# Kernel tuning notes

Hardware: AMD Instinct MI355X
Metric: run time of the kernel (lower is better)

Reference implementation:

```python
import jax, jax.numpy as jnp
import numpy as np

H = 32; L = 4; HEADS = 8; VC = 16; BIG = 1e9

def _unit(v):
    return v * jax.lax.rsqrt(jnp.sum(v * v, -1, keepdims=True) + 1e-8)

def _dihedrals(bb):
    n = bb.shape[0]
    X = bb[:, :3].reshape(n * 3, 3)
    U = _unit(X[1:] - X[:-1])
    u2, u1, u0 = U[:-2], U[1:-1], U[2:]
    n2 = _unit(jnp.cross(u2, u1)); n1 = _unit(jnp.cross(u1, u0))
    cosD = jnp.clip(jnp.sum(n2 * n1, -1), -1 + 1e-6, 1 - 1e-6)
    D = jnp.sign(jnp.sum(u2 * n1, -1)) * jnp.arccos(cosD)
    D = jnp.pad(D, (1, 2)).reshape(n, 3)
    return jnp.concatenate([jnp.cos(D), jnp.sin(D)], -1)

def _orientations(x):
    f = jnp.pad(_unit(x[1:] - x[:-1]), ((0, 1), (0, 0)))
    b = jnp.pad(_unit(x[:-1] - x[1:]), ((1, 0), (0, 0)))
    return jnp.stack([f, b], -2)

def _virtual_cb(bb):
    n_, ca, c = bb[:, 0], bb[:, 1], bb[:, 2]
    b = ca - n_; cc = c - ca; a = jnp.cross(b, cc)
    return -0.58273431 * a + 0.56802827 * b - 0.54067466 * cc + ca

def _rbf(d, nbin=16, dmax=20.0):
    mu = jnp.linspace(0.0, dmax, nbin); sig = dmax / nbin
    return jnp.exp(-(((d[..., None] - mu) / sig) ** 2))

def _pos_emb(didx, nemb=16):
    freq = jnp.exp(jnp.arange(0, nemb, 2, dtype=jnp.float32) * (-np.log(10000.0) / nemb))
    ang = didx[..., None].astype(jnp.float32) * freq
    return jnp.concatenate([jnp.cos(ang), jnp.sin(ang)], -1)

def _edge_rot(vec):
    # per-edge rotation aligning edge direction to e_y (equiformer-style)
    nrm = _unit(vec)
    helper = jnp.where(jnp.abs(nrm[..., 2:3]) > 0.99, jnp.array([1.0, 0.0, 0.0]), jnp.array([0.0, 0.0, 1.0]))
    z = _unit(jnp.cross(nrm, helper))
    x = jnp.cross(nrm, z)
    return jnp.stack([x, nrm, z], axis=-2)

def _rot(R, x):
    return jnp.concatenate([x[..., :1, :], jnp.einsum('...ij,...jc->...ic', R, x[..., 1:, :])], -2)

def _rot_inv(R, x):
    return jnp.concatenate([x[..., :1, :], jnp.einsum('...ji,...jc->...ic', R, x[..., 1:, :])], -2)

def _norm_so3(x, g0, b0, g1):
    x0 = x[..., 0, :]; x1 = x[..., 1:, :]
    mu = jnp.mean(x0, -1, keepdims=True)
    var = jnp.var(x0, -1, keepdims=True)
    y0 = (x0 - mu) * jax.lax.rsqrt(var + 1e-6) * g0 + b0
    y1 = x1 * jax.lax.rsqrt(jnp.mean(x1 * x1, (-2, -1), keepdims=True) + 1e-6) * g1
    return jnp.concatenate([y0[..., None, :], y1], -2)

def _project(xin, nbr, R, ef, rw1, rw2, ow):
    src = _rot(R, xin[nbr])                         # [N,k,4,Cin] gather + rotate into edge frame
    rad = jax.nn.silu(ef @ rw1) @ rw2               # [N,k,Cin] radial weights
    msg = _rot_inv(R, src * rad[..., None, :])      # rotate back to global frame
    return jnp.mean(msg, axis=1) @ ow               # [N,4,Cout]

def _forward(bb, latent, ln_g0, ln_b0, ln_g1, bb_rad_w1, bb_rad_w2, bb_out_w,
             lat_rad_w1, lat_rad_w2, lat_out_w, tln_g0, tln_b0, tln_g1,
             attn_w1, attn_w2, v_w, o_w, ffn_w1, ffn_w2, ffn_wg, ffn_v1,
             eu_w1, eu_w2, out_rad_w1, out_rad_w2, out_w,
             seq_w1, seq_b1, seq_w2, seq_b2, seq_w3, seq_b3, x_mask, n_per, k):
    N = bb.shape[0]
    Xca = bb[:, 1]
    # backbone SO3 features [N,4,7]: l=0 dihedrals (padded to 7), l=1 seven vectors
    dih = jnp.pad(_dihedrals(bb), ((0, 0), (0, 1)))
    vecs = jnp.concatenate([bb - Xca[:, None], _orientations(Xca),
                            (_virtual_cb(bb) - Xca)[:, None]], -2)
    bb_feat = jnp.concatenate([dih[:, None, :], jnp.nan_to_num(jnp.swapaxes(vecs, -1, -2))], 1)
    # kNN graph within each chain; masked residues pushed far away
    batch = jnp.arange(N) // n_per
    mx = jnp.where(x_mask[:, None], BIG, Xca)
    sq = jnp.sum(mx * mx, -1)
    d2 = sq[:, None] + sq[None, :] - 2.0 * (mx @ mx.T)
    bad = (batch[:, None] != batch[None, :]) | jnp.eye(N, dtype=bool)
    d2 = jnp.where(bad, BIG, d2)
    _, nbr = jax.lax.top_k(-d2, k)                  # [N,k] source indices per target
    edge_vec = Xca[:, None] - Xca[nbr]
    R = _edge_rot(edge_vec)                         # [N,k,3,3]
    dist = jnp.sqrt(jnp.sum(edge_vec * edge_vec, -1) + 1e-12)
    ef = jnp.concatenate([_rbf(dist), _pos_emb(nbr - jnp.arange(N)[:, None])], -1)  # [N,k,32]
    lat = _norm_so3(latent, ln_g0, ln_b0, ln_g1)
    x = jnp.concatenate([_project(bb_feat, nbr, R, ef, bb_rad_w1, bb_rad_w2, bb_out_w),
                         _project(lat, nbr, R, ef, lat_rad_w1, lat_rad_w2, lat_out_w)], -1)  # [N,4,H]
    for l in range(L):
        xl = _norm_so3(x, tln_g0[l], tln_b0[l], tln_g1[l])
        src = xl[nbr]                               # [N,k,4,H]
        feat = jnp.concatenate([src[..., 0, :],
                                jnp.broadcast_to(xl[:, None, 0, :], src[..., 0, :].shape),
                                ef], -1)            # [N,k,3H]
        alpha = jax.nn.softmax(jax.nn.silu(feat @ attn_w1[l]) @ attn_w2[l], axis=1)  # [N,k,heads]
        v = _rot_inv(R, _rot(R, src) @ v_w[l])      # [N,k,4,heads*vc]
        v = v.reshape(N, k, 4, HEADS, VC)
        agg = jnp.einsum('nkh,nkchv->nchv', alpha, v).reshape(N, 4, HEADS * VC)
        x = x + agg @ o_w[l]
        h = jax.nn.silu(x[:, 0, :] @ ffn_w1[l])
        gate = jax.nn.sigmoid(h @ ffn_wg[l])
        x = x + jnp.concatenate([(h @ ffn_w2[l])[:, None, :],
                                 (x[:, 1:, :] @ ffn_v1[l]) * gate[:, None, :]], 1)
        e_in = jnp.concatenate([ef, x[nbr][..., 0, :],
                                jnp.broadcast_to(x[:, None, 0, :], (N, k, H))], -1)
        ef = ef + jax.nn.silu(e_in @ eu_w1[l]) @ eu_w2[l]
    atoms = _project(x, nbr, R, ef, out_rad_w1, out_rad_w2, out_w)  # [N,4,91]
    decoded_latent = jnp.swapaxes(atoms[:, 1:4, :], -1, -2)         # [N,91,3]
    hh = jax.nn.relu(x[:, 0, :] @ seq_w1 + seq_b1)
    hh = jax.nn.relu(hh @ seq_w2 + seq_b2)
    seq_logits = jax.nn.log_softmax(hh @ seq_w3 + seq_b3, -1)
    return decoded_latent, seq_logits

def setup_inputs() -> dict:
    key = jax.random.key(0)
    N = 8192; n_per = 2048; k = 30
    keys = iter(jax.random.split(key, 64))
    def W(shape):
        fan = shape[-2] if len(shape) > 1 else shape[-1]
        return (jax.random.normal(next(keys), shape) / np.sqrt(fan)).astype(jnp.float32)
    inp = {
        'bb': (jax.random.normal(next(keys), (N, 4, 3)) * 3.0).astype(jnp.float32),
        'latent': jax.random.normal(next(keys), (N, 4, H), dtype=jnp.float32),
        'ln_g0': jnp.ones((H,), jnp.float32), 'ln_b0': jnp.zeros((H,), jnp.float32), 'ln_g1': jnp.ones((H,), jnp.float32),
        'bb_rad_w1': W((H, 64)), 'bb_rad_w2': W((64, 7)), 'bb_out_w': W((7, 16)),
        'lat_rad_w1': W((H, 64)), 'lat_rad_w2': W((64, H)), 'lat_out_w': W((H, 16)),
        'tln_g0': jnp.ones((L, H), jnp.float32), 'tln_b0': jnp.zeros((L, H), jnp.float32), 'tln_g1': jnp.ones((L, H), jnp.float32),
        'attn_w1': W((L, 3 * H, H)), 'attn_w2': W((L, H, HEADS)),
        'v_w': W((L, H, HEADS * VC)), 'o_w': W((L, HEADS * VC, H)),
        'ffn_w1': W((L, H, 2 * H)), 'ffn_w2': W((L, 2 * H, H)), 'ffn_wg': W((L, 2 * H, H)), 'ffn_v1': W((L, H, H)),
        'eu_w1': W((L, 3 * H, 2 * H)), 'eu_w2': W((L, 2 * H, H)),
        'out_rad_w1': W((H, 64)), 'out_rad_w2': W((64, H)), 'out_w': W((H, 91)),
        'seq_w1': W((H, 64)), 'seq_b1': jnp.zeros((64,), jnp.float32),
        'seq_w2': W((64, H)), 'seq_b2': jnp.zeros((H,), jnp.float32),
        'seq_w3': W((H, 20)), 'seq_b3': jnp.zeros((20,), jnp.float32),
        'x_mask': jnp.zeros((N,), bool), 'n_per': n_per, 'k': k,
    }
    return inp

def reference(bb, latent, ln_g0, ln_b0, ln_g1, bb_rad_w1, bb_rad_w2, bb_out_w,
              lat_rad_w1, lat_rad_w2, lat_out_w, tln_g0, tln_b0, tln_g1,
              attn_w1, attn_w2, v_w, o_w, ffn_w1, ffn_w2, ffn_wg, ffn_v1,
              eu_w1, eu_w2, out_rad_w1, out_rad_w2, out_w,
              seq_w1, seq_b1, seq_w2, seq_b2, seq_w3, seq_b3, x_mask, n_per, k):
    return _forward(bb, latent, ln_g0, ln_b0, ln_g1, bb_rad_w1, bb_rad_w2, bb_out_w,
                    lat_rad_w1, lat_rad_w2, lat_out_w, tln_g0, tln_b0, tln_g1,
                    attn_w1, attn_w2, v_w, o_w, ffn_w1, ffn_w2, ffn_wg, ffn_v1,
                    eu_w1, eu_w2, out_rad_w1, out_rad_w2, out_w,
                    seq_w1, seq_b1, seq_w2, seq_b2, seq_w3, seq_b3, x_mask, n_per, k)
```

## Files before the change

### kernel.cpp

```cpp
#include <hip/hip_runtime.h>
#include <math.h>

#define NRES 8192
#define NPER 2048
#define KNB  30
#define NEDGE (NRES*KNB)

typedef float v2f __attribute__((ext_vector_type(2)));

__device__ __forceinline__ float siluf(float x){ return x / (1.0f + __expf(-x)); }
__device__ __forceinline__ v2f splat2(float a){ v2f r; r.x=a; r.y=a; return r; }

__global__ void k_bbfeat(const float* __restrict__ bb, float* __restrict__ bbf,
                         float4* __restrict__ ca){
  int n = blockIdx.x*256 + threadIdx.x;
  if(n >= NRES) return;
  const float* r = bb + n*12;
  float cax=r[3], cay=r[4], caz=r[5];
  ca[n] = make_float4(cax,cay,caz, cax*cax+cay*cay+caz*caz);
  float vx[7],vy[7],vz[7];
  for(int a=0;a<4;a++){ vx[a]=r[a*3]-cax; vy[a]=r[a*3+1]-cay; vz[a]=r[a*3+2]-caz; }
  if(n<NRES-1){
    float dx=bb[(n+1)*12+3]-cax, dy=bb[(n+1)*12+4]-cay, dz=bb[(n+1)*12+5]-caz;
    float s=rsqrtf(dx*dx+dy*dy+dz*dz+1e-8f);
// ... 83 lines not shown
    if(j==il) d2 = 1e30f;
    vals[t]=d2;
  }
  unsigned mask = 0;
  unsigned long long s0 = knn_extract(vals, mask, lane);
  unsigned long long s1 = knn_extract(vals, mask, lane);
  unsigned long long s2 = knn_extract(vals, mask, lane);
  unsigned long long s3 = knn_extract(vals, mask, lane);
  const unsigned long long EMPTY = ~0ull;
  for(int it=0; it<KNB; it++){
    unsigned long long m = s0;
    #pragma unroll
    for(int off=32; off>0; off>>=1){
      unsigned long long o = __shfl_xor(m, off, 64);
      m = (o<m) ? o : m;
    }
    if(lane==0) nbr[i*KNB+it] = base + (int)(m & 0x7FFull);
    if((int)(m & 63ull) == lane){
      s0=s1; s1=s2; s2=s3; s3=EMPTY;
      if(s0==EMPTY) s0 = knn_extract(vals, mask, lane);
    }
  }
}

__global__ void k_tbl(float* __restrict__ tbl){
  int i = blockIdx.x*256 + threadIdx.x;
  int d = i>>3, m = i&7;
  float freq = __expf(-1.1512925465f*(float)m);
  float ang = (float)(d-2048)*freq;
  tbl[d*16+m]   = cosf(ang);
  tbl[d*16+8+m] = sinf(ang);
}

__global__ void k_edgefeat(const float4* __restrict__ ca, const int* __restrict__ nbr,
                           const float* __restrict__ tbl, float* __restrict__ ef){
  int e = blockIdx.x*256 + threadIdx.x;
  if(e >= NEDGE) return;
  int n = e/KNB;
  int j = nbr[e];
  float4 cn = ca[n], cj = ca[j];
  float dx=cn.x-cj.x, dy=cn.y-cj.y, dz=cn.z-cj.z;
  float dist = sqrtf(dx*dx+dy*dy+dz*dz + 1e-12f);
  float f[32];
  #pragma unroll
  for(int m=0;m<16;m++){
    float mu = (20.0f/15.0f)*(float)m;
    float t = (dist-mu)*(1.0f/1.25f);
    f[m] = __expf(-t*t);
  }
  {
    const float4* t4 = (const float4*)(tbl + (size_t)(j - n + 2048)*16);
    float4 c0=t4[0], c1=t4[1], s0=t4[2], s1=t4[3];
    f[16]=c0.x; f[17]=c0.y; f[18]=c0.z; f[19]=c0.w;
    f[20]=c1.x; f[21]=c1.y; f[22]=c1.z; f[23]=c1.w;
    f[24]=s0.x; f[25]=s0.y; f[26]=s0.z; f[27]=s0.w;
    f[28]=s1.x; f[29]=s1.y; f[30]=s1.z; f[31]=s1.w;
  }
  float4* o4 = (float4*)(ef + (size_t)e*32);
  #pragma unroll
  for(int q=0;q<8;q++) o4[q] = make_float4(f[q*4],f[q*4+1],f[q*4+2],f[q*4+3]);
}

__global__ void k_norm(const float* __restrict__ in, float* __restrict__ out,
                       const float* __restrict__ g0, const float* __restrict__ b0,
                       const float* __restrict__ g1){
  int tid = blockIdx.x*256 + threadIdx.x;
  int n = tid >> 5, lane = tid & 31;
  if(n >= NRES) return;
  const float* xn = in + n*128;
  float x0 = xn[lane];
  float s = x0, s2 = x0*x0;
  for(int off=16; off>0; off>>=1){ s += __shfl_xor(s, off, 32); s2 += __shfl_xor(s2, off, 32); }
  float mu = s*(1.0f/32.0f);
  float var = s2*(1.0f/32.0f) - mu*mu;
  float y0 = (x0-mu)*rsqrtf(var+1e-6f)*g0[lane] + b0[lane];
  float v1 = xn[32+lane], v2 = xn[64+lane], v3 = xn[96+lane];
  float ss = v1*v1+v2*v2+v3*v3;
  for(int off=16; off>0; off>>=1){ ss += __shfl_xor(ss, off, 32); }
  float sc = rsqrtf(ss*(1.0f/96.0f) + 1e-6f);
  float g = g1[lane];
  out[n*128+lane]     = y0;
  out[n*128+32+lane]  = v1*sc*g;
  out[n*128+64+lane]  = v2*sc*g;
  out[n*128+96+lane]  = v3*sc*g;
}

__device__ __forceinline__ void load32(float* __restrict__ f, const float* __restrict__ src){
  const float4* s4 = (const float4*)src;
  #pragma unroll
  for(int q=0;q<8;q++){
    float4 v = s4[q];
    f[q*4+0]=v.x; f[q*4+1]=v.y; f[q*4+2]=v.z; f[q*4+3]=v.w;
  }
}

__global__ __launch_bounds__(128, 4)
void k_rad(const float* __restrict__ ef,
           const float* __restrict__ bbw1, const float* __restrict__ bbw2,
           const float* __restrict__ latw1, const float* __restrict__ latw2,
           float* __restrict__ radbb, float* __restrict__ radlat){
  int e = blockIdx.x*128 + threadIdx.x;
  float f[32];
  load32(f, ef + (size_t)e*32);
  float ab[7];
  #pragma unroll
  for(int t=0;t<7;t++) ab[t]=0.f;
  #pragma unroll
  for(int half=0; half<2; half++){
    v2f h[16];
    #pragma unroll
    for(int o=0;o<16;o++) h[o]=splat2(0.f);
    #pragma unroll
    for(int c=0;c<32;c++){
      v2f fc = splat2(f[c]);
      const v2f* w = (const v2f*)(bbw1 + c*64 + half*32);
      #pragma unroll
      for(int o=0;o<16;o++) h[o] += fc*w[o];
    }
    #pragma unroll
    for(int o=0;o<16;o++){
      float v0 = siluf(h[o].x), v1 = siluf(h[o].y);
      const float* wa = bbw2 + (half*32+o*2)*7;
      const float* wb = bbw2 + (half*32+o*2+1)*7;
      #pragma unroll
      for(int t=0;t<7;t++) ab[t] += v0*wa[t];
      #pragma unroll
      for(int t=0;t<7;t++) ab[t] += v1*wb[t];
    }
  }
  {
    float4* rb4 = (float4*)(radbb + (size_t)e*8);
    rb4[0] = make_float4(ab[0],ab[1],ab[2],ab[3]);
    rb4[1] = make_float4(ab[4],ab[5],ab[6],0.f);
  }
  v2f al[16];
  #pragma unroll
  for(int t=0;t<16;t++) al[t]=splat2(0.f);
  #pragma unroll
  for(int half=0; half<2; half++){
    v2f h[16];
    #pragma unroll
    for(int o=0;o<16;o++) h[o]=splat2(0.f);
    #pragma unroll
    for(int c=0;c<32;c++){
      v2f fc = splat2(f[c]);
      const v2f* w = (const v2f*)(latw1 + c*64 + half*32);
      #pragma unroll
      for(int o=0;o<16;o++) h[o] += fc*w[o];
    }
    #pragma unroll
    for(int o=0;o<16;o++){
      float v0 = siluf(h[o].x), v1 = siluf(h[o].y);
      const v2f* wa = (const v2f*)(latw2 + (half*32+o*2)*32);
      const v2f* wb = (const v2f*)(latw2 + (half*32+o*2+1)*32);
      v2f va = splat2(v0), vb = splat2(v1);
      #pragma unroll
      for(int t=0;t<16;t++) al[t] += va*wa[t];
      #pragma unroll
      for(int t=0;t<16;t++) al[t] += vb*wb[t];
    }
  }
  v2f* rl2 = (v2f*)(radlat + (size_t)e*32);
  #pragma unroll
  for(int q=0;q<16;q++) rl2[q] = al[q];
}

__global__ __launch_bounds__(256) void k_init(const int* __restrict__ nbr,
                       const float* __restrict__ radbb, const float* __restrict__ radlat,
                       const float* __restrict__ bbf, const float* __restrict__ latn,
                       const float* __restrict__ bboutw, const float* __restrict__ latoutw,
                       const float* __restrict__ g0, const float* __restrict__ b0,
                       const float* __restrict__ g1,
                       float* __restrict__ x, float* __restrict__ xl){
  __shared__ float msgbb[4][32], msglat[4][128], xout[4][128];
  int g = threadIdx.x>>6, t = threadIdx.x&63;
  int n = blockIdx.x*4 + g;
  int t31 = t&31, t7 = t%7;
  float accL0=0.f, accL1=0.f, accB=0.f;
  for(int kk=0; kk<KNB; kk++){
    int e = n*KNB+kk;
    int j = nbr[e];
    float rl = radlat[(size_t)e*32 + t31];
    accL0 += latn[j*128+t]    * rl;
    accL1 += latn[j*128+64+t] * rl;
    if(t<28) accB += bbf[j*28+t]*radbb[(size_t)e*8 + t7];
  }
  msglat[g][t]=accL0*(1.0f/KNB); msglat[g][64+t]=accL1*(1.0f/KNB);
  if(t<28) msgbb[g][t]=accB*(1.0f/KNB);
  for(int half=0; half<2; half++){
    int e = half*64+t;
    int rrow = e>>5, c = e&31;
    float v=0.f;
    if(c<16){ for(int q=0;q<7;q++)  v += msgbb[g][rrow*7+q]*bboutw[q*16+c]; }
    else    { for(int q=0;q<32;q++) v += msglat[g][rrow*32+q]*latoutw[q*16+(c-16)]; }
    xout[g][e]=v;
    x[n*128+e]=v;
  }
  if(t<32){
    float x0=xout[g][t];
    float s=x0, s2=x0*x0;
    for(int off=16; off>0; off>>=1){ s+=__shfl_xor(s,off,32); s2+=__shfl_xor(s2,off,32); }
    float mu=s*(1.0f/32.0f), var=s2*(1.0f/32.0f)-mu*mu;
    float y0=(x0-mu)*rsqrtf(var+1e-6f)*g0[t]+b0[t];
    float v1=xout[g][32+t], v2=xout[g][64+t], v3=xout[g][96+t];
    float ss=v1*v1+v2*v2+v3*v3;
    for(int off=16; off>0; off>>=1) ss+=__shfl_xor(ss,off,32);
    float sc=rsqrtf(ss*(1.0f/96.0f)+1e-6f);
    float gg=g1[t];
    xl[n*128+t]=y0; xl[n*128+32+t]=v1*sc*gg; xl[n*128+64+t]=v2*sc*gg; xl[n*128+96+t]=v3*sc*gg;
  }
}

__global__ __launch_bounds__(256) void k_nodeprep(const float* __restrict__ x,
                       const float* __restrict__ xl,
                       const float* __restrict__ ew1, const float* __restrict__ aw1,
                       float* __restrict__ hsrc, float* __restrict__ hdst,
                       float* __restrict__ asrc, float* __restrict__ adst){
  __shared__ float sx[4][32], sl[4][32];
  int g = threadIdx.x>>6, lane = threadIdx.x&63;
  int n = blockIdx.x*4 + g;
  if(lane<32){
    if(x)   sx[g][lane] = x[n*128+lane];
    if(aw1) sl[g][lane] = xl[n*128+lane];
  }
  __syncthreads();
  if(x){
    float a0=0.f, a1=0.f;
    #pragma unroll
    for(int c=0;c<32;c++){
      float xv = sx[g][c];
      a0 += xv*ew1[(32+c)*64+lane];
      a1 += xv*ew1[(64+c)*64+lane];
    }
    hsrc[n*64+lane]=a0; hdst[n*64+lane]=a1;
  }
  if(aw1){
    int o = lane&31;
    int roff = (lane>=32)? 32 : 0;
    float a=0.f;
    #pragma unroll
    for(int c=0;c<32;c++) a += sl[g][c]*aw1[(roff+c)*32+o];
    if(lane<32) asrc[n*32+o]=a; else adst[n*32+o]=a;
  }
}

__global__ __launch_bounds__(128, 4)
void k_logits(const int* __restrict__ nbr,
              const float* __restrict__ asrc, const float* __restrict__ adst,
              const float* __restrict__ ef, const float* __restrict__ w1,
              const float* __restrict__ w2, float* __restrict__ logits){
  int e = blockIdx.x*128 + threadIdx.x;
  int n = e/KNB;
  int j = nbr[e];
  v2f h[16];
  {
    const v2f* pj = (const v2f*)(asrc + (size_t)j*32);
    const v2f* pn = (const v2f*)(adst + (size_t)n*32);
    #pragma unroll
    for(int q=0;q<16;q++) h[q] = pj[q]+pn[q];
  }
  float f[32];
  load32(f, ef + (size_t)e*32);
  #pragma unroll
  for(int c=0;c<32;c++){
    v2f fc = splat2(f[c]);
    const v2f* w = (const v2f*)(w1 + (64+c)*32);
    #pragma unroll
    for(int o=0;o<16;o++) h[o] += fc*w[o];
  }
  v2f acc[4];
  #pragma unroll
  for(int t=0;t<4;t++) acc[t]=splat2(0.f);
  #pragma unroll
  for(int o=0;o<16;o++){
    float v0 = siluf(h[o].x), v1 = siluf(h[o].y);
    const v2f* wa = (const v2f*)(w2 + (o*2)*8);
    const v2f* wb = (const v2f*)(w2 + (o*2+1)*8);
    v2f va = splat2(v0), vb = splat2(v1);
    #pragma unroll
    for(int t=0;t<4;t++) acc[t] += va*wa[t];
    #pragma unroll
    for(int t=0;t<4;t++) acc[t] += vb*wb[t];
  }
  v2f* lg2 = (v2f*)(logits + (size_t)e*8);
  #pragma unroll
  for(int q=0;q<4;q++) lg2[q] = acc[q];
}

__global__ __launch_bounds__(256) void k_update(const int* __restrict__ nbr, const float* __restrict__ xl,
                         const float* __restrict__ logits, float* __restrict__ x,
                         float* __restrict__ xlout,
                         const float* __restrict__ vw, const float* __restrict__ ow,
                         const float* __restrict__ fw1, const float* __restrict__ fw2,
                         const float* __restrict__ fwg, const float* __restrict__ fv1,
                         const float* __restrict__ g0, const float* __restrict__ b0,
                         const float* __restrict__ g1){
  __shared__ float S_lg[4][240], S_m[4][8], S_inv[4][8];
  __shared__ float S_S[4][1024], S_agg[4][512], S_x[4][128];
  __shared__ float S_h[4][64], S_g[4][32], S_d0[4][32];
  int g = threadIdx.x>>6, t = threadIdx.x&63;
  int n = blockIdx.x*4 + g;
  for(int r=t; r<240; r+=64) S_lg[g][r] = logits[(size_t)n*240+r];
  if(t<8){
    float m=-1e30f;
    for(int kk=0;kk<KNB;kk++) m=fmaxf(m, S_lg[g][kk*8+t]);
    float s=0.f;
    for(int kk=0;kk<KNB;kk++) s += __expf(S_lg[g][kk*8+t]-m);
    S_m[g][t]=m; S_inv[g][t]=1.0f/s;
  }
  for(int r=t; r<240; r+=64){ int h=r&7; S_lg[g][r]=__expf(S_lg[g][r]-S_m[g][h])*S_inv[g][h]; }
  int hd = t>>3, i8 = t&7;
  v2f acc[8];
  #pragma unroll
  for(int m=0;m<8;m++) acc[m]=splat2(0.f);
  for(int kk=0;kk<KNB;kk++){
    int j=nbr[n*KNB+kk];
    v2f a = splat2(S_lg[g][kk*8+hd]);
    const v2f* xr = (const v2f*)(xl + (size_t)j*128 + i8*16);
    #pragma unroll
    for(int q=0;q<8;q++) acc[q] += a*xr[q];
  }
  #pragma unroll
  for(int q=0;q<8;q++){ S_S[g][hd*128 + i8*16 + 2*q] = acc[q].x; S_S[g][hd*128 + i8*16 + 2*q+1] = acc[q].y; }
  __syncthreads();
  for(int half=0; half<2; half++){
    int hv = half*64+t;
    int hh = hv>>4;
    v2f a01=splat2(0.f), a23=splat2(0.f);
    for(int c=0;c<32;c++){
      v2f w = splat2(vw[c*128+hv]);
      v2f s01; s01.x = S_S[g][hh*128 + c];      s01.y = S_S[g][hh*128 + 32+c];
      v2f s23; s23.x = S_S[g][hh*128 + 64+c];   s23.y = S_S[g][hh*128 + 96+c];
      a01 += s01*w; a23 += s23*w;
    }
    S_agg[g][hv]=a01.x; S_agg[g][128+hv]=a01.y; S_agg[g][256+hv]=a23.x; S_agg[g][384+hv]=a23.y;
  }
  __syncthreads();
  {
    int c = t&31, r0 = t>>5;
    v2f v01; v01.x = x[n*128+t]; v01.y = x[n*128+64+t];
    for(int hv=0;hv<128;hv++){
      v2f s; s.x = S_agg[g][r0*128+hv]; s.y = S_agg[g][(r0+2)*128+hv];
      v01 += s*splat2(ow[hv*32+c]);
    }
    S_x[g][t]=v01.x; S_x[g][64+t]=v01.y;
  }
  __syncthreads();
  {
    float hs=0.f;
    for(int c=0;c<32;c++) hs += S_x[g][c]*fw1[c*64+t];
    S_h[g][t]=siluf(hs);
  }
  __syncthreads();
  if(t<32){
    float gs=0.f, d0=0.f;
    for(int c=0;c<64;c++){ float hv=S_h[g][c]; gs += hv*fwg[c*32+t]; d0 += hv*fw2[c*32+t]; }
    S_g[g][t]=1.0f/(1.0f+__expf(-gs));
    S_d0[g][t]=d0;
  }
  __syncthreads();
  for(int half=0; half<2; half++){
    int e = half*64+t;
    int rrow = e>>5, c = e&31;
    float xv = S_x[g][e], outv;
    if(rrow==0){ outv = xv + S_d0[g][c]; }
    else {
      float dv=0.f;
      for(int cc=0;cc<32;cc++) dv += S_x[g][rrow*32+cc]*fv1[cc*32+c];
      outv = xv + dv*S_g[g][c];
    }
    __syncthreads();
    S_x[g][e]=outv;
    x[n*128+e]=outv;
  }
  __syncthreads();
  if(t<32){
    float x0=S_x[g][t];
    float s=x0, s2=x0*x0;
    for(int off=16; off>0; off>>=1){ s+=__shfl_xor(s,off,32); s2+=__shfl_xor(s2,off,32); }
    float mu=s*(1.0f/32.0f), var=s2*(1.0f/32.0f)-mu*mu;
    float y0=(x0-mu)*rsqrtf(var+1e-6f)*g0[t]+b0[t];
    float v1=S_x[g][32+t], v2=S_x[g][64+t], v3=S_x[g][96+t];
    float ss=v1*v1+v2*v2+v3*v3;
    for(int off=16; off>0; off>>=1) ss+=__shfl_xor(ss,off,32);
    float sc=rsqrtf(ss*(1.0f/96.0f)+1e-6f);
    float gg=g1[t];
    xlout[n*128+t]=y0; xlout[n*128+32+t]=v1*sc*gg;
    xlout[n*128+64+t]=v2*sc*gg; xlout[n*128+96+t]=v3*sc*gg;
  }
}

template<bool FUSE_LOGITS>
__global__ __launch_bounds__(128, 4)
void k_efup_t(const int* __restrict__ nbr,
              const float* __restrict__ hsrc, const float* __restrict__ hdst,
              const float* __restrict__ ew1, const float* __restrict__ ew2,
              float* __restrict__ ef,
              const float* __restrict__ asrc, const float* __restrict__ adst,
              const float* __restrict__ aw1n, const float* __restrict__ aw2n,
              float* __restrict__ logits){
  int e = blockIdx.x*128 + threadIdx.x;
  int n = e/KNB;
  int j = nbr[e];
  float f[32];
  load32(f, ef + (size_t)e*32);
  v2f acc[16];
  #pragma unroll
  for(int t=0;t<16;t++) acc[t]=splat2(0.f);
  #pragma unroll
  for(int half=0; half<2; half++){
    v2f h[16];
    {
      const v2f* pj = (const v2f*)(hsrc + (size_t)j*64 + half*32);
      const v2f* pn = (const v2f*)(hdst + (size_t)n*64 + half*32);
      #pragma unroll
      for(int q=0;q<16;q++) h[q] = pj[q]+pn[q];
    }
    #pragma unroll
    for(int c=0;c<32;c++){
      v2f fc = splat2(f[c]);
      const v2f* w = (const v2f*)(ew1 + c*64 + half*32);
      #pragma unroll
      for(int o=0;o<16;o++) h[o] += fc*w[o];
    }
    #pragma unroll
    for(int o=0;o<16;o++){
      float v0 = siluf(h[o].x), v1 = siluf(h[o].y);
      const v2f* wa = (const v2f*)(ew2 + (half*32+o*2)*32);
      const v2f* wb = (const v2f*)(ew2 + (half*32+o*2+1)*32);
      v2f va = splat2(v0), vb = splat2(v1);
      #pragma unroll
      for(int t=0;t<16;t++) acc[t] += va*wa[t];
      #pragma unroll
      for(int t=0;t<16;t++) acc[t] += vb*wb[t];
    }
  }
  #pragma unroll
  for(int t=0;t<16;t++){ f[2*t] += acc[t].x; f[2*t+1] += acc[t].y; }
  float4* e4 = (float4*)(ef + (size_t)e*32);
  #pragma unroll
  for(int q=0;q<8;q++)
    e4[q] = make_float4(f[q*4+0], f[q*4+1], f[q*4+2], f[q*4+3]);
  if(FUSE_LOGITS){
    v2f h2[16];
    {
      const v2f* pj = (const v2f*)(asrc + (size_t)j*32);
      const v2f* pn = (const v2f*)(adst + (size_t)n*32);
      #pragma unroll
      for(int q=0;q<16;q++) h2[q] = pj[q]+pn[q];
    }
    #pragma unroll
    for(int c=0;c<32;c++){
      v2f fc = splat2(f[c]);
      const v2f* w = (const v2f*)(aw1n + (64+c)*32);
      #pragma unroll
      for(int o=0;o<16;o++) h2[o] += fc*w[o];
    }
    v2f a8[4];
    #pragma unroll
    for(int t=0;t<4;t++) a8[t]=splat2(0.f);
    #pragma unroll
    for(int o=0;o<16;o++){
      float v0 = siluf(h2[o].x), v1 = siluf(h2[o].y);
      const v2f* wa = (const v2f*)(aw2n + (o*2)*8);
      const v2f* wb = (const v2f*)(aw2n + (o*2+1)*8);
      v2f va = splat2(v0), vb = splat2(v1);
      #pragma unroll
      for(int t=0;t<4;t++) a8[t] += va*wa[t];
      #pragma unroll
      for(int t=0;t<4;t++) a8[t] += vb*wb[t];
    }
    v2f* lg2 = (v2f*)(logits + (size_t)e*8);
    #pragma unroll
    for(int q=0;q<4;q++) lg2[q] = a8[q];
  }
}

__global__ __launch_bounds__(128, 4)
void k_orad(const float* __restrict__ ef,
            const float* __restrict__ orw1, const float* __restrict__ orw2,
            float* __restrict__ orad){
  int e = blockIdx.x*128 + threadIdx.x;
  float f[32];
  load32(f, ef + (size_t)e*32);
  v2f acc[16];
  #pragma unroll
  for(int t=0;t<16;t++) acc[t]=splat2(0.f);
  #pragma unroll
  for(int half=0; half<2; half++){
    v2f h[16];
    #pragma unroll
    for(int o=0;o<16;o++) h[o]=splat2(0.f);
    #pragma unroll
    for(int c=0;c<32;c++){
      v2f fc = splat2(f[c]);
      const v2f* w = (const v2f*)(orw1 + c*64 + half*32);
      #pragma unroll
      for(int o=0;o<16;o++) h[o] += fc*w[o];
    }
    #pragma unroll
    for(int o=0;o<16;o++){
      float v0 = siluf(h[o].x), v1 = siluf(h[o].y);
      const v2f* wa = (const v2f*)(orw2 + (half*32+o*2)*32);
      const v2f* wb = (const v2f*)(orw2 + (half*32+o*2+1)*32);
      v2f va = splat2(v0), vb = splat2(v1);
      #pragma unroll
      for(int t=0;t<16;t++) acc[t] += va*wa[t];
      #pragma unroll
      for(int t=0;t<16;t++) acc[t] += vb*wb[t];
    }
  }
  v2f* r2 = (v2f*)(orad + (size_t)e*32);
  #pragma unroll
  for(int q=0;q<16;q++) r2[q] = acc[q];
}

__global__ __launch_bounds__(256) void k_out(const int* __restrict__ nbr, const float* __restrict__ orad,
                      const float* __restrict__ x,
                      const float* __restrict__ outw,
                      const float* __restrict__ sw1, const float* __restrict__ sb1,
                      const float* __restrict__ sw2, const float* __restrict__ sb2,
                      const float* __restrict__ sw3, const float* __restrict__ sb3,
                      float* __restrict__ out, float* __restrict__ outseq){
  __shared__ float msg[4][128];
  __shared__ float h1[4][64], h2[4][32], lgs[4][20];
  int g = threadIdx.x>>6, t = threadIdx.x&63;
  int n = blockIdx.x*4 + g;
  int t31 = t&31;
  float acc0=0.f, acc1=0.f;
  for(int kk=0;kk<KNB;kk++){
    int e=n*KNB+kk;
    int j=nbr[e];
    float rl = orad[(size_t)e*32 + t31];
    acc0 += x[j*128+t]*rl;
    acc1 += x[j*128+64+t]*rl;
  }
  msg[g][t]=acc0*(1.0f/KNB); msg[g][64+t]=acc1*(1.0f/KNB);
  for(int o=t;o<91;o+=64){
    for(int rrow=1;rrow<4;rrow++){
      float s=0.f;
      for(int c=0;c<32;c++) s += msg[g][rrow*32+c]*outw[c*91+o];
      out[(size_t)n*273 + o*3 + (rrow-1)] = s;
    }
  }
  {
    float s=0.f;
    for(int c=0;c<32;c++) s += x[n*128+c]*sw1[c*64+t];
// ... 37 lines not shown
  const float* tg1     = (const float*)d_in[13];
  const float* aw1     = (const float*)d_in[14];
  const float* aw2     = (const float*)d_in[15];
  const float* vw      = (const float*)d_in[16];
  const float* ow      = (const float*)d_in[17];
  const float* fw1     = (const float*)d_in[18];
  const float* fw2     = (const float*)d_in[19];
  const float* fwg     = (const float*)d_in[20];
  const float* fv1     = (const float*)d_in[21];
  const float* ew1     = (const float*)d_in[22];
  const float* ew2     = (const float*)d_in[23];
  const float* orw1    = (const float*)d_in[24];
  const float* orw2    = (const float*)d_in[25];
  const float* outw    = (const float*)d_in[26];
  const float* sw1     = (const float*)d_in[27];
  const float* sb1     = (const float*)d_in[28];
  const float* sw2     = (const float*)d_in[29];
  const float* sb2     = (const float*)d_in[30];
  const float* sw3     = (const float*)d_in[31];
  const float* sb3     = (const float*)d_in[32];
  float* outp = (float*)d_out;

  int*    nbr    = (int*)d_ws;
  float*  ef     = (float*)((char*)d_ws + 1024*1024);
  float*  xbuf   = ef   + (size_t)NEDGE*32;
  float*  xlA    = xbuf + (size_t)NRES*128;
  float*  xlB    = xlA  + (size_t)NRES*128;
  float*  bbf    = xlB  + (size_t)NRES*128;
  float*  logits = bbf  + (size_t)NRES*28;
  float4* ca     = (float4*)(logits + (size_t)NEDGE*8);
  float*  edgescratch = (float*)(ca + NRES);
  float*  radbb  = logits;
  float*  radlat = edgescratch;
  float*  orad   = edgescratch;
  float*  tbl    = edgescratch;
  float*  hsrc   = edgescratch;
  float*  hdst   = edgescratch + (size_t)NRES*64;
  float*  asrc   = edgescratch + (size_t)NRES*128;
  float*  adst   = edgescratch + (size_t)NRES*128 + (size_t)NRES*32;

  k_bbfeat  <<<NRES/256, 256, 0, stream>>>(bb, bbf, ca);
  k_knn     <<<NRES/4,   256, 0, stream>>>(ca, nbr);
  k_tbl     <<<4096*8/256, 256, 0, stream>>>(tbl);
  k_edgefeat<<<NEDGE/256, 256, 0, stream>>>(ca, nbr, tbl, ef);
  k_norm    <<<NRES*32/256, 256, 0, stream>>>(latent, xlA, ln_g0, ln_b0, ln_g1);
  k_rad     <<<NEDGE/128, 128, 0, stream>>>(ef, bbw1, bbw2, latw1, latw2, radbb, radlat);
  k_init    <<<NRES/4, 256, 0, stream>>>(nbr, radbb, radlat, bbf, xlA,
                                         bboutw, latoutw,
                                         tg0, tb0, tg1,
                                         xbuf, xlB);
  k_nodeprep<<<NRES/4, 256, 0, stream>>>(nullptr, xlB, ew1, aw1, hsrc, hdst, asrc, adst);
  k_logits  <<<NEDGE/128, 128, 0, stream>>>(nbr, asrc, adst, ef, aw1, aw2, logits);
  for(int l=0;l<4;l++){
    const float* xl_in  = (l&1) ? xlA : xlB;
    float*       xl_out = (l&1) ? xlB : xlA;
    int ln = (l+1<4) ? (l+1) : 3;
    k_update <<<NRES/4, 256, 0, stream>>>(nbr, xl_in, logits, xbuf, xl_out,
                                          vw+l*32*128, ow+l*128*32,
                                          fw1+l*32*64, fw2+l*64*32,
                                          fwg+l*64*32, fv1+l*32*32,
                                          tg0+ln*32, tb0+ln*32, tg1+ln*32);
    if(l<3){
      k_nodeprep<<<NRES/4, 256, 0, stream>>>(xbuf, xl_out, ew1+l*96*64, aw1+(l+1)*96*32,
                                             hsrc, hdst, asrc, adst);
      k_efup_t<true><<<NEDGE/128, 128, 0, stream>>>(nbr, hsrc, hdst,
                                                    ew1+l*96*64, ew2+l*64*32, ef,
                                                    asrc, adst,
                                                    aw1+(l+1)*96*32, aw2+(l+1)*32*8, logits);
    } else {
      k_nodeprep<<<NRES/4, 256, 0, stream>>>(xbuf, xl_out, ew1+l*96*64, nullptr,
                                             hsrc, hdst, asrc, adst);
      k_efup_t<false><<<NEDGE/128, 128, 0, stream>>>(nbr, hsrc, hdst,
                                                     ew1+l*96*64, ew2+l*64*32, ef,
                                                     nullptr, nullptr,
                                                     nullptr, nullptr, nullptr);
    }
  }
  k_orad<<<NEDGE/128, 128, 0, stream>>>(ef, orw1, orw2, orad);
  k_out <<<NRES/4, 256, 0, stream>>>(nbr, orad, xbuf, outw,
                                     sw1, sb1, sw2, sb2, sw3, sb3,
                                     outp, outp + (size_t)NRES*273);
}
```

Baseline: 1.153 ms.

## Fuse edge-feature/radial, node-prep/update and last edge-update/output-radial kernels

Merges k_edgefeat with k_rad so the edge features are used straight from registers, not written out and re-read. Folds the per-node hsrc/hdst/asrc/adst projections into the tail of k_update, which removes the separate k_nodeprep launches per layer. The final k_efup is fused with k_orad and writes the output radial weights into the ef buffer, and the pos-emb table moves into xbuf. k_update also drops its __syncthreads, relying on each 64-thread group being a single wave64 wavefront, and switches to float4 neighbour loads. That reliance on implicit wave-level ordering of LDS accesses is a correctness risk, and the fused kernels may see higher register pressure.

```diff
diff --git a/kernel.cpp b/kernel.cpp
--- a/kernel.cpp
+++ b/kernel.cpp
@@ -139,10 +139,13 @@
   tbl[d*16+8+m] = sinf(ang);
 }
 
-__global__ void k_edgefeat(const float4* __restrict__ ca, const int* __restrict__ nbr,
-                           const float* __restrict__ tbl, float* __restrict__ ef){
-  int e = blockIdx.x*256 + threadIdx.x;
-  if(e >= NEDGE) return;
+__global__ __launch_bounds__(128, 4)
+void k_edgerad(const float4* __restrict__ ca, const int* __restrict__ nbr,
+               const float* __restrict__ tbl,
+               const float* __restrict__ bbw1, const float* __restrict__ bbw2,
+               const float* __restrict__ latw1, const float* __restrict__ latw2,
+               float* __restrict__ ef, float* __restrict__ radbb, float* __restrict__ radlat){
+  int e = blockIdx.x*128 + threadIdx.x;
   int n = e/KNB;
   int j = nbr[e];
   float4 cn = ca[n], cj = ca[j];
@@ -163,9 +166,72 @@
     f[24]=s0.x; f[25]=s0.y; f[26]=s0.z; f[27]=s0.w;
     f[28]=s1.x; f[29]=s1.y; f[30]=s1.z; f[31]=s1.w;
   }
-  float4* o4 = (float4*)(ef + (size_t)e*32);
-  #pragma unroll
-  for(int q=0;q<8;q++) o4[q] = make_float4(f[q*4],f[q*4+1],f[q*4+2],f[q*4+3]);
+  {
+    float4* o4 = (float4*)(ef + (size_t)e*32);
+    #pragma unroll
+    for(int q=0;q<8;q++) o4[q] = make_float4(f[q*4],f[q*4+1],f[q*4+2],f[q*4+3]);
+  }
+  float ab[7];
+  #pragma unroll
+  for(int t=0;t<7;t++) ab[t]=0.f;
+  #pragma unroll
+  for(int half=0; half<2; half++){
+    v2f h[16];
+    #pragma unroll
+    for(int o=0;o<16;o++) h[o]=splat2(0.f);
+    #pragma unroll
+    for(int c=0;c<32;c++){
+      v2f fc = splat2(f[c]);
+      const v2f* w = (const v2f*)(bbw1 + c*64 + half*32);
+      #pragma unroll
+      for(int o=0;o<16;o++) h[o] += fc*w[o];
+    }
+    #pragma unroll
+    for(int o=0;o<16;o++){
+      float v0 = siluf(h[o].x), v1 = siluf(h[o].y);
+      const float* wa = bbw2 + (half*32+o*2)*7;
+      const float* wb = bbw2 + (half*32+o*2+1)*7;
+      #pragma unroll
+      for(int t=0;t<7;t++) ab[t] += v0*wa[t];
+      #pragma unroll
+      for(int t=0;t<7;t++) ab[t] += v1*wb[t];
+    }
+  }
+  {
+    float4* rb4 = (float4*)(radbb + (size_t)e*8);
+    rb4[0] = make_float4(ab[0],ab[1],ab[2],ab[3]);
+    rb4[1] = make_float4(ab[4],ab[5],ab[6],0.f);
+  }
+  v2f al[16];
+  #pragma unroll
+  for(int t=0;t<16;t++) al[t]=splat2(0.f);
+  #pragma unroll
+  for(int half=0; half<2; half++){
+    v2f h[16];
+    #pragma unroll
+    for(int o=0;o<16;o++) h[o]=splat2(0.f);
+    #pragma unroll
+    for(int c=0;c<32;c++){
+      v2f fc = splat2(f[c]);
+      const v2f* w = (const v2f*)(latw1 + c*64 + half*32);
+      #pragma unroll
+      for(int o=0;o<16;o++) h[o] += fc*w[o];
+    }
+    #pragma unroll
+    for(int o=0;o<16;o++){
+      float v0 = siluf(h[o].x), v1 = siluf(h[o].y);
+      const v2f* wa = (const v2f*)(latw2 + (half*32+o*2)*32);
+      const v2f* wb = (const v2f*)(latw2 + (half*32+o*2+1)*32);
+      v2f va = splat2(v0), vb = splat2(v1);
+      #pragma unroll
+      for(int t=0;t<16;t++) al[t] += va*wa[t];
+      #pragma unroll
+      for(int t=0;t<16;t++) al[t] += vb*wb[t];
+    }
+  }
+  v2f* rl2 = (v2f*)(radlat + (size_t)e*32);
+  #pragma unroll
+  for(int q=0;q<16;q++) rl2[q] = al[q];
 }
 
 __global__ void k_norm(const float* __restrict__ in, float* __restrict__ out,
@@ -201,77 +267,6 @@
   }
 }
 
-__global__ __launch_bounds__(128, 4)
-void k_rad(const float* __restrict__ ef,
-           const float* __restrict__ bbw1, const float* __restrict__ bbw2,
-           const float* __restrict__ latw1, const float* __restrict__ latw2,
-           float* __restrict__ radbb, float* __restrict__ radlat){
-  int e = blockIdx.x*128 + threadIdx.x;
-  float f[32];
-  load32(f, ef + (size_t)e*32);
-  float ab[7];
-  #pragma unroll
-  for(int t=0;t<7;t++) ab[t]=0.f;
-  #pragma unroll
-  for(int half=0; half<2; half++){
-    v2f h[16];
-    #pragma unroll
-    for(int o=0;o<16;o++) h[o]=splat2(0.f);
-    #pragma unroll
-    for(int c=0;c<32;c++){
-      v2f fc = splat2(f[c]);
-      const v2f* w = (const v2f*)(bbw1 + c*64 + half*32);
-      #pragma unroll
-      for(int o=0;o<16;o++) h[o] += fc*w[o];
-    }
-    #pragma unroll
-    for(int o=0;o<16;o++){
-      float v0 = siluf(h[o].x), v1 = siluf(h[o].y);
-      const float* wa = bbw2 + (half*32+o*2)*7;
-      const float* wb = bbw2 + (half*32+o*2+1)*7;
-      #pragma unroll
-      for(int t=0;t<7;t++) ab[t] += v0*wa[t];
-      #pragma unroll
-      for(int t=0;t<7;t++) ab[t] += v1*wb[t];
-    }
-  }
-  {
-    float4* rb4 = (float4*)(radbb + (size_t)e*8);
-    rb4[0] = make_float4(ab[0],ab[1],ab[2],ab[3]);
-    rb4[1] = make_float4(ab[4],ab[5],ab[6],0.f);
-  }
-  v2f al[16];
-  #pragma unroll
-  for(int t=0;t<16;t++) al[t]=splat2(0.f);
-  #pragma unroll
-  for(int half=0; half<2; half++){
-    v2f h[16];
-    #pragma unroll
-    for(int o=0;o<16;o++) h[o]=splat2(0.f);
-    #pragma unroll
-    for(int c=0;c<32;c++){
-      v2f fc = splat2(f[c]);
-      const v2f* w = (const v2f*)(latw1 + c*64 + half*32);
-      #pragma unroll
-      for(int o=0;o<16;o++) h[o] += fc*w[o];
-    }
-    #pragma unroll
-    for(int o=0;o<16;o++){
-      float v0 = siluf(h[o].x), v1 = siluf(h[o].y);
-      const v2f* wa = (const v2f*)(latw2 + (half*32+o*2)*32);
-      const v2f* wb = (const v2f*)(latw2 + (half*32+o*2+1)*32);
-      v2f va = splat2(v0), vb = splat2(v1);
-      #pragma unroll
-      for(int t=0;t<16;t++) al[t] += va*wa[t];
-      #pragma unroll
-      for(int t=0;t<16;t++) al[t] += vb*wb[t];
-    }
-  }
-  v2f* rl2 = (v2f*)(radlat + (size_t)e*32);
-  #pragma unroll
-  for(int q=0;q<16;q++) rl2[q] = al[q];
-}
-
 __global__ __launch_bounds__(256) void k_init(const int* __restrict__ nbr,
                        const float* __restrict__ radbb, const float* __restrict__ radlat,
                        const float* __restrict__ bbf, const float* __restrict__ latn,
@@ -318,37 +313,20 @@
   }
 }
 
-__global__ __launch_bounds__(256) void k_nodeprep(const float* __restrict__ x,
-                       const float* __restrict__ xl,
-                       const float* __restrict__ ew1, const float* __restrict__ aw1,
-                       float* __restrict__ hsrc, float* __restrict__ hdst,
+__global__ __launch_bounds__(256) void k_nodeprep0(const float* __restrict__ xl,
+                       const float* __restrict__ aw1,
                        float* __restrict__ asrc, float* __restrict__ adst){
-  __shared__ float sx[4][32], sl[4][32];
+  __shared__ float sl[4][32];
   int g = threadIdx.x>>6, lane = threadIdx.x&63;
   int n = blockIdx.x*4 + g;
-  if(lane<32){
-    if(x)   sx[g][lane] = x[n*128+lane];
-    if(aw1) sl[g][lane] = xl[n*128+lane];
-  }
+  if(lane<32) sl[g][lane] = xl[n*128+lane];
   __syncthreads();
-  if(x){
-    float a0=0.f, a1=0.f;
-    #pragma unroll
-    for(int c=0;c<32;c++){
-      float xv = sx[g][c];
-      a0 += xv*ew1[(32+c)*64+lane];
-      a1 += xv*ew1[(64+c)*64+lane];
-    }
-    hsrc[n*64+lane]=a0; hdst[n*64+lane]=a1;
-  }
-  if(aw1){
-    int o = lane&31;
-    int roff = (lane>=32)? 32 : 0;
-    float a=0.f;
-    #pragma unroll
-    for(int c=0;c<32;c++) a += sl[g][c]*aw1[(roff+c)*32+o];
-    if(lane<32) asrc[n*32+o]=a; else adst[n*32+o]=a;
-  }
+  int o = lane&31;
+  int roff = (lane>=32)? 32 : 0;
+  float a=0.f;
+  #pragma unroll
+  for(int c=0;c<32;c++) a += sl[g][c]*aw1[(roff+c)*32+o];
+  if(lane<32) asrc[n*32+o]=a; else adst[n*32+o]=a;
 }
 
 __global__ __launch_bounds__(128, 4)
@@ -401,10 +379,13 @@
                          const float* __restrict__ fw1, const float* __restrict__ fw2,
                          const float* __restrict__ fwg, const float* __restrict__ fv1,
                          const float* __restrict__ g0, const float* __restrict__ b0,
-                         const float* __restrict__ g1){
+                         const float* __restrict__ g1,
+                         const float* __restrict__ ew1l, const float* __restrict__ aw1n,
+                         float* __restrict__ hsrc, float* __restrict__ hdst,
+                         float* __restrict__ asrc, float* __restrict__ adst){
   __shared__ float S_lg[4][240], S_m[4][8], S_inv[4][8];
   __shared__ float S_S[4][1024], S_agg[4][512], S_x[4][128];
-  __shared__ float S_h[4][64], S_g[4][32], S_d0[4][32];
+  __shared__ float S_h[4][64], S_g[4][32], S_d0[4][32], S_y0[4][32];
   int g = threadIdx.x>>6, t = threadIdx.x&63;
   int n = blockIdx.x*4 + g;
   for(int r=t; r<240; r+=64) S_lg[g][r] = logits[(size_t)n*240+r];
@@ -417,55 +398,53 @@
   }
   for(int r=t; r<240; r+=64){ int h=r&7; S_lg[g][r]=__expf(S_lg[g][r]-S_m[g][h])*S_inv[g][h]; }
   int hd = t>>3, i8 = t&7;
-  v2f acc[8];
-  #pragma unroll
-  for(int m=0;m<8;m++) acc[m]=splat2(0.f);
+  const float4* xl4 = (const float4*)xl;
+  float acc[16];
+  for(int m=0;m<16;m++) acc[m]=0.f;
   for(int kk=0;kk<KNB;kk++){
     int j=nbr[n*KNB+kk];
-    v2f a = splat2(S_lg[g][kk*8+hd]);
-    const v2f* xr = (const v2f*)(xl + (size_t)j*128 + i8*16);
-    #pragma unroll
-    for(int q=0;q<8;q++) acc[q] += a*xr[q];
-  }
-  #pragma unroll
-  for(int q=0;q<8;q++){ S_S[g][hd*128 + i8*16 + 2*q] = acc[q].x; S_S[g][hd*128 + i8*16 + 2*q+1] = acc[q].y; }
-  __syncthreads();
+    float a = S_lg[g][kk*8+hd];
+    float4 b0v = xl4[j*32 + i8*4 + 0];
+    float4 b1v = xl4[j*32 + i8*4 + 1];
+    float4 b2v = xl4[j*32 + i8*4 + 2];
+    float4 b3v = xl4[j*32 + i8*4 + 3];
+    acc[0]+=a*b0v.x; acc[1]+=a*b0v.y; acc[2]+=a*b0v.z; acc[3]+=a*b0v.w;
+    acc[4]+=a*b1v.x; acc[5]+=a*b1v.y; acc[6]+=a*b1v.z; acc[7]+=a*b1v.w;
+    acc[8]+=a*b2v.x; acc[9]+=a*b2v.y; acc[10]+=a*b2v.z; acc[11]+=a*b2v.w;
+    acc[12]+=a*b3v.x; acc[13]+=a*b3v.y; acc[14]+=a*b3v.z; acc[15]+=a*b3v.w;
+  }
+  for(int m=0;m<16;m++) S_S[g][hd*128 + i8*16 + m] = acc[m];
   for(int half=0; half<2; half++){
     int hv = half*64+t;
     int hh = hv>>4;
-    v2f a01=splat2(0.f), a23=splat2(0.f);
+    float a0=0.f,a1=0.f,a2=0.f,a3=0.f;
     for(int c=0;c<32;c++){
-      v2f w = splat2(vw[c*128+hv]);
-      v2f s01; s01.x = S_S[g][hh*128 + c];      s01.y = S_S[g][hh*128 + 32+c];
-      v2f s23; s23.x = S_S[g][hh*128 + 64+c];   s23.y = S_S[g][hh*128 + 96+c];
-      a01 += s01*w; a23 += s23*w;
-    }
-    S_agg[g][hv]=a01.x; S_agg[g][128+hv]=a01.y; S_agg[g][256+hv]=a23.x; S_agg[g][384+hv]=a23.y;
-  }
-  __syncthreads();
-  {
-    int c = t&31, r0 = t>>5;
-    v2f v01; v01.x = x[n*128+t]; v01.y = x[n*128+64+t];
-    for(int hv=0;hv<128;hv++){
-      v2f s; s.x = S_agg[g][r0*128+hv]; s.y = S_agg[g][(r0+2)*128+hv];
-      v01 += s*splat2(ow[hv*32+c]);
-    }
-    S_x[g][t]=v01.x; S_x[g][64+t]=v01.y;
-  }
-  __syncthreads();
+      float w = vw[c*128+hv];
+      a0 += S_S[g][hh*128 + c]*w;
+      a1 += S_S[g][hh*128 + 32+c]*w;
+      a2 += S_S[g][hh*128 + 64+c]*w;
+      a3 += S_S[g][hh*128 + 96+c]*w;
+    }
+    S_agg[g][hv]=a0; S_agg[g][128+hv]=a1; S_agg[g][256+hv]=a2; S_agg[g][384+hv]=a3;
+  }
+  for(int half=0; half<2; half++){
+    int e = half*64+t;
+    int rrow = e>>5, c = e&31;
+    float v = x[n*128+e];
+    for(int hv=0;hv<128;hv++) v += S_agg[g][rrow*128+hv]*ow[hv*32+c];
+    S_x[g][e]=v;
+  }
   {
     float hs=0.f;
     for(int c=0;c<32;c++) hs += S_x[g][c]*fw1[c*64+t];
     S_h[g][t]=siluf(hs);
   }
-  __syncthreads();
   if(t<32){
     float gs=0.f, d0=0.f;
     for(int c=0;c<64;c++){ float hv=S_h[g][c]; gs += hv*fwg[c*32+t]; d0 += hv*fw2[c*32+t]; }
     S_g[g][t]=1.0f/(1.0f+__expf(-gs));
     S_d0[g][t]=d0;
   }
-  __syncthreads();
   for(int half=0; half<2; half++){
     int e = half*64+t;
     int rrow = e>>5, c = e&31;
@@ -476,11 +455,9 @@
       for(int cc=0;cc<32;cc++) dv += S_x[g][rrow*32+cc]*fv1[cc*32+c];
       outv = xv + dv*S_g[g][c];
     }
-    __syncthreads();
     S_x[g][e]=outv;
     x[n*128+e]=outv;
   }
-  __syncthreads();
   if(t<32){
     float x0=S_x[g][t];
     float s=x0, s2=x0*x0;
@@ -494,18 +471,36 @@
     float gg=g1[t];
     xlout[n*128+t]=y0; xlout[n*128+32+t]=v1*sc*gg;
     xlout[n*128+64+t]=v2*sc*gg; xlout[n*128+96+t]=v3*sc*gg;
-  }
-}
-
-template<bool FUSE_LOGITS>
+    S_y0[g][t]=y0;
+  }
+  {
+    float a0=0.f, a1=0.f;
+    #pragma unroll
+    for(int c=0;c<32;c++){
+      float xv = S_x[g][c];
+      a0 += xv*ew1l[(32+c)*64+t];
+      a1 += xv*ew1l[(64+c)*64+t];
+    }
+    hsrc[n*64+t]=a0; hdst[n*64+t]=a1;
+  }
+  if(aw1n){
+    int o = t&31;
+    int roff = (t>=32)? 32 : 0;
+    float a=0.f;
+    #pragma unroll
+    for(int c=0;c<32;c++) a += S_y0[g][c]*aw1n[(roff+c)*32+o];
+    if(t<32) asrc[n*32+o]=a; else adst[n*32+o]=a;
+  }
+}
+
 __global__ __launch_bounds__(128, 4)
-void k_efup_t(const int* __restrict__ nbr,
-              const float* __restrict__ hsrc, const float* __restrict__ hdst,
-              const float* __restrict__ ew1, const float* __restrict__ ew2,
-              float* __restrict__ ef,
-              const float* __restrict__ asrc, const float* __restrict__ adst,
-              const float* __restrict__ aw1n, const float* __restrict__ aw2n,
-              float* __restrict__ logits){
+void k_efup(const int* __restrict__ nbr,
+            const float* __restrict__ hsrc, const float* __restrict__ hdst,
+            const float* __restrict__ ew1, const float* __restrict__ ew2,
+            float* __restrict__ ef,
+            const float* __restrict__ asrc, const float* __restrict__ adst,
+            const float* __restrict__ aw1n, const float* __restrict__ aw2n,
+            float* __restrict__ logits){
   int e = blockIdx.x*128 + threadIdx.x;
   int n = e/KNB;
   int j = nbr[e];
@@ -548,51 +543,86 @@
   #pragma unroll
   for(int q=0;q<8;q++)
     e4[q] = make_float4(f[q*4+0], f[q*4+1], f[q*4+2], f[q*4+3]);
-  if(FUSE_LOGITS){
-    v2f h2[16];
-    {
-      const v2f* pj = (const v2f*)(asrc + (size_t)j*32);
-      const v2f* pn = (const v2f*)(adst + (size_t)n*32);
-      #pragma unroll
-      for(int q=0;q<16;q++) h2[q] = pj[q]+pn[q];
-    }
-    #pragma unroll
-    for(int c=0;c<32;c++){
-      v2f fc = splat2(f[c]);
-      const v2f* w = (const v2f*)(aw1n + (64+c)*32);
-      #pragma unroll
-      for(int o=0;o<16;o++) h2[o] += fc*w[o];
-    }
-    v2f a8[4];
-    #pragma unroll
-    for(int t=0;t<4;t++) a8[t]=splat2(0.f);
-    #pragma unroll
-    for(int o=0;o<16;o++){
-      float v0 = siluf(h2[o].x), v1 = siluf(h2[o].y);
-      const v2f* wa = (const v2f*)(aw2n + (o*2)*8);
-      const v2f* wb = (const v2f*)(aw2n + (o*2+1)*8);
-      v2f va = splat2(v0), vb = splat2(v1);
-      #pragma unroll
-      for(int t=0;t<4;t++) a8[t] += va*wa[t];
-      #pragma unroll
-      for(int t=0;t<4;t++) a8[t] += vb*wb[t];
-    }
-    v2f* lg2 = (v2f*)(logits + (size_t)e*8);
-    #pragma unroll
-    for(int q=0;q<4;q++) lg2[q] = a8[q];
-  }
+  v2f h2[16];
+  {
+    const v2f* pj = (const v2f*)(asrc + (size_t)j*32);
+    const v2f* pn = (const v2f*)(adst + (size_t)n*32);
+    #pragma unroll
+    for(int q=0;q<16;q++) h2[q] = pj[q]+pn[q];
+  }
+  #pragma unroll
+  for(int c=0;c<32;c++){
+    v2f fc = splat2(f[c]);
+    const v2f* w = (const v2f*)(aw1n + (64+c)*32);
+    #pragma unroll
+    for(int o=0;o<16;o++) h2[o] += fc*w[o];
+  }
+  v2f a8[4];
+  #pragma unroll
+  for(int t=0;t<4;t++) a8[t]=splat2(0.f);
+  #pragma unroll
+  for(int o=0;o<16;o++){
+    float v0 = siluf(h2[o].x), v1 = siluf(h2[o].y);
+    const v2f* wa = (const v2f*)(aw2n + (o*2)*8);
+    const v2f* wb = (const v2f*)(aw2n + (o*2+1)*8);
+    v2f va = splat2(v0), vb = splat2(v1);
+    #pragma unroll
+    for(int t=0;t<4;t++) a8[t] += va*wa[t];
+    #pragma unroll
+    for(int t=0;t<4;t++) a8[t] += vb*wb[t];
+  }
+  v2f* lg2 = (v2f*)(logits + (size_t)e*8);
+  #pragma unroll
+  for(int q=0;q<4;q++) lg2[q] = a8[q];
 }
 
 __global__ __launch_bounds__(128, 4)
-void k_orad(const float* __restrict__ ef,
-            const float* __restrict__ orw1, const float* __restrict__ orw2,
-            float* __restrict__ orad){
+void k_efup_orad(const int* __restrict__ nbr,
+                 const float* __restrict__ hsrc, const float* __restrict__ hdst,
+                 const float* __restrict__ ew1, const float* __restrict__ ew2,
+                 float* __restrict__ ef,
+                 const float* __restrict__ orw1, const float* __restrict__ orw2){
   int e = blockIdx.x*128 + threadIdx.x;
+  int n = e/KNB;
+  int j = nbr[e];
   float f[32];
   load32(f, ef + (size_t)e*32);
   v2f acc[16];
   #pragma unroll
   for(int t=0;t<16;t++) acc[t]=splat2(0.f);
+  #pragma unroll
+  for(int half=0; half<2; half++){
+    v2f h[16];
+    {
+      const v2f* pj = (const v2f*)(hsrc + (size_t)j*64 + half*32);
+      const v2f* pn = (const v2f*)(hdst + (size_t)n*64 + half*32);
+      #pragma unroll
+      for(int q=0;q<16;q++) h[q] = pj[q]+pn[q];
+    }
+    #pragma unroll
+    for(int c=0;c<32;c++){
+      v2f fc = splat2(f[c]);
+      const v2f* w = (const v2f*)(ew1 + c*64 + half*32);
+      #pragma unroll
+      for(int o=0;o<16;o++) h[o] += fc*w[o];
+    }
+    #pragma unroll
+    for(int o=0;o<16;o++){
+      float v0 = siluf(h[o].x), v1 = siluf(h[o].y);
+      const v2f* wa = (const v2f*)(ew2 + (half*32+o*2)*32);
+      const v2f* wb = (const v2f*)(ew2 + (half*32+o*2+1)*32);
+      v2f va = splat2(v0), vb = splat2(v1);
+      #pragma unroll
+      for(int t=0;t<16;t++) acc[t] += va*wa[t];
+      #pragma unroll
+      for(int t=0;t<16;t++) acc[t] += vb*wb[t];
+    }
+  }
+  #pragma unroll
+  for(int t=0;t<16;t++){ f[2*t] += acc[t].x; f[2*t+1] += acc[t].y; }
+  v2f oa[16];
+  #pragma unroll
+  for(int t=0;t<16;t++) oa[t]=splat2(0.f);
   #pragma unroll
   for(int half=0; half<2; half++){
     v2f h[16];
@@ -612,14 +642,14 @@
       const v2f* wb = (const v2f*)(orw2 + (half*32+o*2+1)*32);
       v2f va = splat2(v0), vb = splat2(v1);
       #pragma unroll
-      for(int t=0;t<16;t++) acc[t] += va*wa[t];
-      #pragma unroll
-      for(int t=0;t<16;t++) acc[t] += vb*wb[t];
-    }
-  }
-  v2f* r2 = (v2f*)(orad + (size_t)e*32);
-  #pragma unroll
-  for(int q=0;q<16;q++) r2[q] = acc[q];
+      for(int t=0;t<16;t++) oa[t] += va*wa[t];
+      #pragma unroll
+      for(int t=0;t<16;t++) oa[t] += vb*wb[t];
+    }
+  }
+  v2f* r2 = (v2f*)(ef + (size_t)e*32);
+  #pragma unroll
+  for(int q=0;q<16;q++) r2[q] = oa[q];
 }
 
 __global__ __launch_bounds__(256) void k_out(const int* __restrict__ nbr, const float* __restrict__ orad,
@@ -723,8 +753,7 @@
   float*  edgescratch = (float*)(ca + NRES);
   float*  radbb  = logits;
   float*  radlat = edgescratch;
-  float*  orad   = edgescratch;
-  float*  tbl    = edgescratch;
+  float*  tbl    = xbuf;
   float*  hsrc   = edgescratch;
   float*  hdst   = edgescratch + (size_t)NRES*64;
   float*  asrc   = edgescratch + (size_t)NRES*128;
@@ -733,42 +762,39 @@
   k_bbfeat  <<<NRES/256, 256, 0, stream>>>(bb, bbf, ca);
   k_knn     <<<NRES/4,   256, 0, stream>>>(ca, nbr);
   k_tbl     <<<4096*8/256, 256, 0, stream>>>(tbl);
-  k_edgefeat<<<NEDGE/256, 256, 0, stream>>>(ca, nbr, tbl, ef);
+  k_edgerad <<<NEDGE/128, 128, 0, stream>>>(ca, nbr, tbl, bbw1, bbw2, latw1, latw2,
+                                            ef, radbb, radlat);
   k_norm    <<<NRES*32/256, 256, 0, stream>>>(latent, xlA, ln_g0, ln_b0, ln_g1);
-  k_rad     <<<NEDGE/128, 128, 0, stream>>>(ef, bbw1, bbw2, latw1, latw2, radbb, radlat);
   k_init    <<<NRES/4, 256, 0, stream>>>(nbr, radbb, radlat, bbf, xlA,
                                          bboutw, latoutw,
                                          tg0, tb0, tg1,
                                          xbuf, xlB);
-  k_nodeprep<<<NRES/4, 256, 0, stream>>>(nullptr, xlB, ew1, aw1, hsrc, hdst, asrc, adst);
-  k_logits  <<<NEDGE/128, 128, 0, stream>>>(nbr, asrc, adst, ef, aw1, aw2, logits);
+  k_nodeprep0<<<NRES/4, 256, 0, stream>>>(xlB, aw1, asrc, adst);
+  k_logits   <<<NEDGE/128, 128, 0, stream>>>(nbr, asrc, adst, ef, aw1, aw2, logits);
   for(int l=0;l<4;l++){
     const float* xl_in  = (l&1) ? xlA : xlB;
     float*       xl_out = (l&1) ? xlB : xlA;
     int ln = (l+1<4) ? (l+1) : 3;
+    const float* aw1n = (l<3) ? (aw1+(l+1)*96*32) : nullptr;
     k_update <<<NRES/4, 256, 0, stream>>>(nbr, xl_in, logits, xbuf, xl_out,
                                           vw+l*32*128, ow+l*128*32,
                                           fw1+l*32*64, fw2+l*64*32,
                                           fwg+l*64*32, fv1+l*32*32,
-                                          tg0+ln*32, tb0+ln*32, tg1+ln*32);
+                                          tg0+ln*32, tb0+ln*32, tg1+ln*32,
+                                          ew1+l*96*64, aw1n,
+                                          hsrc, hdst, asrc, adst);
     if(l<3){
-      k_nodeprep<<<NRES/4, 256, 0, stream>>>(xbuf, xl_out, ew1+l*96*64, aw1+(l+1)*96*32,
-                                             hsrc, hdst, asrc, adst);
-      k_efup_t<true><<<NEDGE/128, 128, 0, stream>>>(nbr, hsrc, hdst,
-                                                    ew1+l*96*64, ew2+l*64*32, ef,
-                                                    asrc, adst,
-                                                    aw1+(l+1)*96*32, aw2+(l+1)*32*8, logits);
+      k_efup<<<NEDGE/128, 128, 0, stream>>>(nbr, hsrc, hdst,
+                                            ew1+l*96*64, ew2+l*64*32, ef,
+                                            asrc, adst,
+                                            aw1+(l+1)*96*32, aw2+(l+1)*32*8, logits);
     } else {
-      k_nodeprep<<<NRES/4, 256, 0, stream>>>(xbuf, xl_out, ew1+l*96*64, nullptr,
-                                             hsrc, hdst, asrc, adst);
-      k_efup_t<false><<<NEDGE/128, 128, 0, stream>>>(nbr, hsrc, hdst,
-                                                     ew1+l*96*64, ew2+l*64*32, ef,
-                                                     nullptr, nullptr,
-                                                     nullptr, nullptr, nullptr);
-    }
-  }
-  k_orad<<<NEDGE/128, 128, 0, stream>>>(ef, orw1, orw2, orad);
-  k_out <<<NRES/4, 256, 0, stream>>>(nbr, orad, xbuf, outw,
+      k_efup_orad<<<NEDGE/128, 128, 0, stream>>>(nbr, hsrc, hdst,
+                                                 ew1+l*96*64, ew2+l*64*32, ef,
+                                                 orw1, orw2);
+    }
+  }
+  k_out <<<NRES/4, 256, 0, stream>>>(nbr, ef , xbuf, outw,
                                      sw1, sb1, sw2, sb2, sw3, sb3,
                                      outp, outp + (size_t)NRES*273);
 }
```

New measurement: 1.210 ms. +4.9%, slower.
